# Kernel optimization log

Hardware: AMD Instinct MI355X
Metric: run time of the kernel (lower is better)

The kernel has to match this reference:

```python
import jax, jax.numpy as jnp
import numpy as np

N_NODES = 50000
N_EDGES = 800000
NFEAT = 128
NHID = 128
NCLASS = 10
NUM_GRAPHS = 512


def setup_inputs() -> dict:
    key = jax.random.key(0)
    ks = jax.random.split(key, 12)
    x = jax.random.normal(ks[0], (N_NODES, NFEAT), dtype=jnp.float32)
    edge_index = jax.random.randint(ks[1], (2, N_EDGES), 0, N_NODES, dtype=jnp.int64)
    batch = jnp.sort(jax.random.randint(ks[2], (N_NODES,), 0, NUM_GRAPHS, dtype=jnp.int64))
    def glorot(k, fan_in, fan_out):
        lim = np.sqrt(6.0 / (fan_in + fan_out))
        return jax.random.uniform(k, (fan_in, fan_out), jnp.float32, -lim, lim)
    return {
        "x": x, "edge_index": edge_index, "batch": batch,
        "W0": glorot(ks[3], NFEAT, NHID), "b0": jnp.zeros((NHID,), jnp.float32),
        "W1": glorot(ks[4], NHID, NHID), "b1": jnp.zeros((NHID,), jnp.float32),
        "W2": glorot(ks[5], NHID, NHID), "b2": jnp.zeros((NHID,), jnp.float32),
        "lin_w": glorot(ks[6], NHID, NCLASS), "lin_b": jnp.zeros((NCLASS,), jnp.float32),
    }


def _gcn_norm(edge_index, n):
    # PyG GCNConv: add self-loops, symmetric normalization D^-1/2 A D^-1/2
    loop = jnp.arange(n, dtype=edge_index.dtype)
    src = jnp.concatenate([edge_index[0], loop])  # [E+N]
    dst = jnp.concatenate([edge_index[1], loop])
    deg = jax.ops.segment_sum(jnp.ones_like(dst, dtype=jnp.float32), dst, num_segments=n)
    dis = jnp.where(deg > 0, jax.lax.rsqrt(jnp.maximum(deg, 1.0)), 0.0)
    norm = dis[src] * dis[dst]  # [E+N]
    return src, dst, norm


def _gcn_conv(x, W, b, src, dst, norm, n):
    h = x @ W                              # [N, nhid]
    msg = h[src] * norm[:, None]           # gather + scale, [E+N, nhid]
    out = jax.ops.segment_sum(msg, dst, num_segments=n)
    return out + b


def reference(x, edge_index, batch, W0, b0, W1, b1, W2, b2, lin_w, lin_b):
    n = x.shape[0]
    src, dst, norm = _gcn_norm(edge_index, n)
    h = x
    for (W, b) in ((W0, b0), (W1, b1), (W2, b2)):
        h = jax.nn.relu(_gcn_conv(h, W, b, src, dst, norm, n))
    # global mean pool over graphs
    sums = jax.ops.segment_sum(h, batch, num_segments=NUM_GRAPHS)
    cnts = jax.ops.segment_sum(jnp.ones((n,), jnp.float32), batch, num_segments=NUM_GRAPHS)
    pooled = sums / jnp.maximum(cnts, 1.0)[:, None]  # [G, nhid]
    logits = pooled @ lin_w + lin_b
    return jax.nn.log_softmax(logits, axis=-1)
```

## Files before the change

kernel.cpp:

```cpp
#include <hip/hip_runtime.h>
#include <hip/hip_fp16.h>


#define FEAT 128
#define NCLASS 10
#define NB_MAX 512

typedef _Float16 h8 __attribute__((ext_vector_type(8)));
typedef float f4 __attribute__((ext_vector_type(4)));

__device__ inline int swz(int row, int cbyte) { return row * 256 + (cbyte ^ ((row & 7) << 4)); }

__global__ void __launch_bounds__(256) prep_kernel(const int* __restrict__ ei,
                                                   int* __restrict__ bhist,
                                                   int ne, int nb, int epb, int hb,
                                                   const float* __restrict__ W0,
                                                   const float* __restrict__ W1,
                                                   const float* __restrict__ W2,
                                                   _Float16* __restrict__ Wt, int wtb,
                                                   const int* __restrict__ batch,
                                                   int* __restrict__ gstart, int n, int g) {
  int t = threadIdx.x;
  if (blockIdx.x >= hb + wtb) {
    int i = (blockIdx.x - hb - wtb) * 256 + t;
    if (i >= n) return;
    int bi = batch[i];
    int bp = (i == 0) ? -1 : batch[i - 1];
    for (int q = bp + 1; q <= bi; ++q) gstart[q] = i;
    if (i == n - 1)
      for (int q = bi + 1; q <= g; ++q) gstart[q] = n;
    return;
  }
  if (blockIdx.x >= hb) {
    int i = (blockIdx.x - hb) * 256 + t;
    if (i < 3 * FEAT * FEAT) {
      int l = i / (FEAT * FEAT);
      int r = i - l * (FEAT * FEAT);
      int nn = r >> 7, kk = r & 127;
      const float* W = (l == 0) ? W0 : (l == 1) ? W1 : W2;
      Wt[i] = (_Float16)W[kk * FEAT + nn];
    }
    return;
  }
  __shared__ int lh[NB_MAX];
  for (int i = t; i < nb; i += 256) lh[i] = 0;
  __syncthreads();
  int r0 = blockIdx.x * epb;
  int r1 = min(r0 + epb, ne);
  for (int k = r0 + t; k < r1; k += 256) atomicAdd(&lh[ei[ne + k] >> 7], 1);
  __syncthreads();
  for (int i = t; i < nb; i += 256)
    if (lh[i]) atomicAdd(&bhist[i], lh[i]);
}

__global__ void __launch_bounds__(512) bscan_kernel(const int* __restrict__ bhist,
                                                    int* __restrict__ bstart,
                                                    int* __restrict__ bcur,
                                                    int nb, int ne) {
  __shared__ int sh[512];
  int t = threadIdx.x;
  int v = (t < nb) ? bhist[t] : 0;
  sh[t] = v;
  __syncthreads();
  int x = v;
  for (int d = 1; d < 512; d <<= 1) {
    int y = (t >= d) ? sh[t - d] : 0;
    __syncthreads();
    x += y;
    sh[t] = x;
    __syncthreads();
  }
  if (t < nb) {
    bstart[t] = x - v;
    bcur[t] = x - v;
  }
  if (t == 0) bstart[nb] = ne;
}

__global__ void __launch_bounds__(256) scatter_kernel(const int* __restrict__ ei,
                                                      int* __restrict__ bcur,
                                                      unsigned* __restrict__ buf,
                                                      int ne, int nb, int epb) {
  __shared__ int lh[NB_MAX], lbs[NB_MAX];
  int t = threadIdx.x;
  for (int i = t; i < nb; i += 256) lh[i] = 0;
  __syncthreads();
  int r0 = blockIdx.x * epb;
  int r1 = min(r0 + epb, ne);
  for (int k = r0 + t; k < r1; k += 256) atomicAdd(&lh[ei[ne + k] >> 7], 1);
  __syncthreads();
  for (int i = t; i < nb; i += 256) {
    int c = lh[i];
    lbs[i] = c ? atomicAdd(&bcur[i], c) : 0;
    lh[i] = 0;
  }
  __syncthreads();
  for (int k = r0 + t; k < r1; k += 256) {
    int src = ei[k];
    int dst = ei[ne + k];
    int b = dst >> 7;
    int p = lbs[b] + atomicAdd(&lh[b], 1);
    buf[p] = (unsigned)src | ((unsigned)(dst & 127) << 25);
  }
}

__global__ void __launch_bounds__(256) bucket_build_kernel(const unsigned* __restrict__ buf,
                                                           const int* __restrict__ bstart,
                                                           int4* __restrict__ off4,
                                                           int* __restrict__ oend,
                                                           int* __restrict__ csr,
                                                           float* __restrict__ dis,
                                                           int n, int csize) {
  __shared__ int cnt[512], cur[512], loc[512], sh[128];
  int b = blockIdx.x, t = threadIdx.x;
  int e0 = bstart[b], e1 = bstart[b + 1];
  int pb = ((e0 + 7) & ~7) + 2048 * b;
  for (int i = t; i < 512; i += 256) cnt[i] = 0;
  __syncthreads();
  for (int k = e0 + t; k < e1; k += 256) {
    unsigned u = buf[k];
    int src = (int)(u & 0x1FFFFFFu);
    int d = u >> 25;
    int c = (src >= 3 * csize) ? 3 : (src >= 2 * csize) ? 2 : (src >= csize) ? 1 : 0;
    atomicAdd(&cnt[d * 4 + c], 1);
  }
  __syncthreads();
  int tot = 0;
  if (t < 128) {
    int p0 = (cnt[t * 4 + 0] + 3) & ~3;
    int p1 = (cnt[t * 4 + 1] + 3) & ~3;
    int p2 = (cnt[t * 4 + 2] + 3) & ~3;
    int p3 = (cnt[t * 4 + 3] + 3) & ~3;
    loc[t * 4 + 0] = 0;
    loc[t * 4 + 1] = p0;
    loc[t * 4 + 2] = p0 + p1;
    loc[t * 4 + 3] = p0 + p1 + p2;
    tot = p0 + p1 + p2 + p3;
    sh[t] = tot;
  }
  __syncthreads();
  int x = tot;
  for (int d = 1; d < 128; d <<= 1) {
    int y = (t < 128 && t >= d) ? sh[t - d] : 0;
    __syncthreads();
    if (t < 128) {
      x += y;
      sh[t] = x;
    }
    __syncthreads();
  }
  if (t < 128) {
    int st = pb + x - tot;
    int node = (b << 7) + t;
    int s0 = st + loc[t * 4 + 0], s1 = st + loc[t * 4 + 1];
    int s2 = st + loc[t * 4 + 2], s3 = st + loc[t * 4 + 3];
    cur[t * 4 + 0] = s0;
    cur[t * 4 + 1] = s1;
    cur[t * 4 + 2] = s2;
    cur[t * 4 + 3] = s3;
    if (node < n) {
      off4[node] = make_int4(s0, s1, s2, s3);
      oend[node] = st + tot;
      int v = cnt[t * 4] + cnt[t * 4 + 1] + cnt[t * 4 + 2] + cnt[t * 4 + 3];
      dis[node] = rsqrtf((float)(v + 1));
    }
  }
  __syncthreads();
  for (int k = e0 + t; k < e1; k += 256) {
    unsigned u = buf[k];
    int src = (int)(u & 0x1FFFFFFu);
    int d = u >> 25;
    int c = (src >= 3 * csize) ? 3 : (src >= 2 * csize) ? 2 : (src >= csize) ? 1 : 0;
    int p = atomicAdd(&cur[d * 4 + c], 1);
    csr[p] = src;
  }
  __syncthreads();
  if (t < 128) {
#pragma unroll
    for (int c = 0; c < 4; ++c) {
      int k0 = t * 4 + c;
      int pad = ((cnt[k0] + 3) & ~3) - cnt[k0];
      int base = cur[k0];
      for (int q = 0; q < pad; ++q) csr[base + q] = n;
    }
  }
}

__global__ void __launch_bounds__(256) gemm_mfma_kernel(const float* __restrict__ Xf,
                                                        const _Float16* __restrict__ Wt,
                                                        const float* __restrict__ dis,
                                                        _Float16* __restrict__ Hs, int n) {
  __shared__ _Float16 st[64 * FEAT];
  int tid = threadIdx.x;
  int w = tid >> 6, lane = tid & 63;
  int l15 = lane & 15, hi = lane >> 4;

  int rowA = blockIdx.x * 64 + w * 16 + l15;
  int rA = min(rowA, n - 1);

  f4 acc[8];
#pragma unroll
  for (int nb = 0; nb < 8; ++nb) acc[nb] = (f4)(0.f);

#pragma unroll
  for (int kk = 0; kk < FEAT; kk += 32) {
    int ko = kk + hi * 8;
    h8 a;
    float4 x0 = *(const float4*)&Xf[(size_t)rA * FEAT + ko];
    float4 x1 = *(const float4*)&Xf[(size_t)rA * FEAT + ko + 4];
    a[0] = (_Float16)x0.x; a[1] = (_Float16)x0.y; a[2] = (_Float16)x0.z; a[3] = (_Float16)x0.w;
    a[4] = (_Float16)x1.x; a[5] = (_Float16)x1.y; a[6] = (_Float16)x1.z; a[7] = (_Float16)x1.w;
#pragma unroll
    for (int nb = 0; nb < 8; ++nb) {
      h8 bfr = *(const h8*)&Wt[(nb * 16 + l15) * FEAT + ko];
      acc[nb] = __builtin_amdgcn_mfma_f32_16x16x32_f16(a, bfr, acc[nb], 0, 0, 0);
    }
  }

  float dv[4];
#pragma unroll
  for (int r = 0; r < 4; ++r) {
    int grow = blockIdx.x * 64 + w * 16 + hi * 4 + r;
    dv[r] = dis[min(grow, n - 1)];
  }
#pragma unroll
  for (int nb = 0; nb < 8; ++nb)
#pragma unroll
    for (int r = 0; r < 4; ++r)
      st[(w * 16 + hi * 4 + r) * FEAT + nb * 16 + l15] = (_Float16)(acc[nb][r] * dv[r]);
  __syncthreads();

  int rowbase = blockIdx.x * 64;
#pragma unroll
  for (int i = tid; i < 64 * FEAT / 8; i += 256) {
    int row = rowbase + (i >> 4);
    if (row < n)
      *(uint4*)&Hs[(size_t)row * FEAT + (i & 15) * 8] =
          *(const uint4*)&st[(i >> 4) * FEAT + (i & 15) * 8];
  }
}

__global__ void __launch_bounds__(512, 6) fused_kernel(const h8* __restrict__ Hs_in,
                                                       const int* __restrict__ csr,
                                                       const int4* __restrict__ off4,
                                                       const int* __restrict__ oend,
                                                       const float* __restrict__ dis,
                                                       const float* __restrict__ bias,
                                                       const _Float16* __restrict__ Wt,
                                                       _Float16* __restrict__ Hs_out, int n) {
  __shared__ char xsb[64 * 256];
  int tid = threadIdx.x;
  int w = tid >> 6, lane = tid & 63;
  int grp = lane >> 4, lig = lane & 15;
  int row0 = blockIdx.x * 64;
  int g32 = w * 4 + grp;

  int nd0 = min(row0 + g32 * 2, n - 1);
  int nd1 = min(row0 + g32 * 2 + 1, n - 1);
  int4 o0 = off4[nd0], o1 = off4[nd1];
  int oe0 = oend[nd0], oe1 = oend[nd1];

  float acc0[8], acc1[8];
  h8 sv0 = Hs_in[(size_t)nd0 * 16 + lig];
  h8 sv1 = Hs_in[(size_t)nd1 * 16 + lig];
#pragma unroll
  for (int j = 0; j < 8; ++j) {
    acc0[j] = (float)sv0[j];
    acc1[j] = (float)sv1[j];
  }

#pragma unroll
  for (int c = 0; c < 4; ++c) {
    int s0 = (c == 0) ? o0.x : (c == 1) ? o0.y : (c == 2) ? o0.z : o0.w;
    int e0 = (c == 0) ? o0.y : (c == 1) ? o0.z : (c == 2) ? o0.w : oe0;
    for (int k = s0; k < e0; k += 4) {
      int4 ci = *(const int4*)&csr[k];
      h8 v0 = Hs_in[(size_t)ci.x * 16 + lig];
      h8 v1 = Hs_in[(size_t)ci.y * 16 + lig];
      h8 v2 = Hs_in[(size_t)ci.z * 16 + lig];
      h8 v3 = Hs_in[(size_t)ci.w * 16 + lig];
#pragma unroll
      for (int j = 0; j < 8; ++j)
        acc0[j] += ((float)v0[j] + (float)v1[j]) + ((float)v2[j] + (float)v3[j]);
    }
    int s1 = (c == 0) ? o1.x : (c == 1) ? o1.y : (c == 2) ? o1.z : o1.w;
    int e1 = (c == 0) ? o1.y : (c == 1) ? o1.z : (c == 2) ? o1.w : oe1;
    for (int k = s1; k < e1; k += 4) {
      int4 ci = *(const int4*)&csr[k];
      h8 v0 = Hs_in[(size_t)ci.x * 16 + lig];
      h8 v1 = Hs_in[(size_t)ci.y * 16 + lig];
      h8 v2 = Hs_in[(size_t)ci.z * 16 + lig];
      h8 v3 = Hs_in[(size_t)ci.w * 16 + lig];
#pragma unroll
      for (int j = 0; j < 8; ++j)
        acc1[j] += ((float)v0[j] + (float)v1[j]) + ((float)v2[j] + (float)v3[j]);
    }
    __syncthreads();
  }

  float d0 = dis[nd0], d1 = dis[nd1];
  float4 bb0 = ((const float4*)bias)[lig * 2];
  float4 bb1 = ((const float4*)bias)[lig * 2 + 1];
  float bb[8] = {bb0.x, bb0.y, bb0.z, bb0.w, bb1.x, bb1.y, bb1.z, bb1.w};
  h8 oA, oB;
#pragma unroll
  for (int j = 0; j < 8; ++j) {
    oA[j] = (_Float16)fmaxf(fmaf(d0, acc0[j], bb[j]), 0.f);
    oB[j] = (_Float16)fmaxf(fmaf(d1, acc1[j], bb[j]), 0.f);
  }
  *(h8*)(xsb + swz(g32 * 2, lig * 16)) = oA;
  *(h8*)(xsb + swz(g32 * 2 + 1, lig * 16)) = oB;
  __syncthreads();

  int l15 = lane & 15, hi = lane >> 4;
  int strip = w & 3, ch = w >> 2;
  f4 acc[4];
#pragma unroll
  for (int nb = 0; nb < 4; ++nb) acc[nb] = (f4)(0.f);
#pragma unroll
  for (int kk = 0; kk < FEAT; kk += 32) {
    int ko = kk + hi * 8;
    h8 a = *(const h8*)(xsb + swz(strip * 16 + l15, ko * 2));
#pragma unroll
    for (int nb = 0; nb < 4; ++nb) {
      h8 bfr = *(const h8*)&Wt[(ch * 64 + nb * 16 + l15) * FEAT + ko];
      acc[nb] = __builtin_amdgcn_mfma_f32_16x16x32_f16(a, bfr, acc[nb], 0, 0, 0);
    }
  }

  float dv[4];
#pragma unroll
  for (int r = 0; r < 4; ++r) {
    int grow = row0 + strip * 16 + hi * 4 + r;
    dv[r] = dis[min(grow, n - 1)];
  }
  __syncthreads();
#pragma unroll
  for (int nb = 0; nb < 4; ++nb)
#pragma unroll
    for (int r = 0; r < 4; ++r) {
      int srow = strip * 16 + hi * 4 + r;
      *(_Float16*)(xsb + swz(srow, (ch * 64 + nb * 16 + l15) * 2)) =
          (_Float16)(acc[nb][r] * dv[r]);
    }
  __syncthreads();
#pragma unroll
  for (int i = tid; i < 64 * FEAT / 8; i += 512) {
    int row = row0 + (i >> 4);
    if (row < n)
      *(uint4*)&Hs_out[(size_t)row * FEAT + (i & 15) * 8] =
          *(const uint4*)(xsb + swz(i >> 4, (i & 15) * 16));
  }
}

__global__ void __launch_bounds__(512, 6) agg_kernel(const h8* __restrict__ Hs,
                                                     const int* __restrict__ csr,
                                                     const int4* __restrict__ off4,
                                                     const int* __restrict__ oend,
                                                     const float* __restrict__ dis,
                                                     const float* __restrict__ bias,
                                                     h8* __restrict__ out, int n) {
  int tid = threadIdx.x;
  int g32 = tid >> 4, lig = tid & 15;
  int row0 = blockIdx.x * 64;

  float4 bb0 = ((const float4*)bias)[lig * 2];
  float4 bb1 = ((const float4*)bias)[lig * 2 + 1];
  float bb[8] = {bb0.x, bb0.y, bb0.z, bb0.w, bb1.x, bb1.y, bb1.z, bb1.w};

#pragma unroll
  for (int m = 0; m < 2; ++m) {
    int node = row0 + g32 * 2 + m;
    int nd = min(node, n - 1);
    int s = off4[nd].x;
    int e = oend[nd];
    float a0[8], a1[8];
    h8 sv = Hs[(size_t)nd * 16 + lig];
#pragma unroll
    for (int j = 0; j < 8; ++j) {
      a0[j] = (float)sv[j];
      a1[j] = 0.f;
    }
    for (int k = s; k < e; k += 4) {
      int4 ci = *(const int4*)&csr[k];
      h8 v0 = Hs[(size_t)ci.x * 16 + lig];
      h8 v1 = Hs[(size_t)ci.y * 16 + lig];
      h8 v2 = Hs[(size_t)ci.z * 16 + lig];
      h8 v3 = Hs[(size_t)ci.w * 16 + lig];
#pragma unroll
      for (int j = 0; j < 8; ++j) a0[j] += (float)v0[j] + (float)v2[j];
#pragma unroll
      for (int j = 0; j < 8; ++j) a1[j] += (float)v1[j] + (float)v3[j];
    }
    float d = dis[nd];
    h8 o;
#pragma unroll
    for (int j = 0; j < 8; ++j)
      o[j] = (_Float16)fmaxf(fmaf(d, a0[j] + a1[j], bb[j]), 0.f);
    if (node < n) out[(size_t)node * 16 + lig] = o;
  }
}

__global__ void __launch_bounds__(128) pool_kernel(const __half* __restrict__ h,
                                                   const int* __restrict__ gstart,
                                                   const float* __restrict__ lw,
                                                   const float* __restrict__ lb,
                                                   float* __restrict__ out) {
  int g = blockIdx.x;
  int t = threadIdx.x;
  int s = gstart[g];
  int e = gstart[g + 1];
  float a0 = 0.f, a1 = 0.f, a2 = 0.f, a3 = 0.f;
  int i = s;
  for (; i + 4 <= e; i += 4) {
    a0 += __half2float(h[(size_t)i * FEAT + t]);
    a1 += __half2float(h[(size_t)(i + 1) * FEAT + t]);
    a2 += __half2float(h[(size_t)(i + 2) * FEAT + t]);
    a3 += __half2float(h[(size_t)(i + 3) * FEAT + t]);
  }
  for (; i < e; ++i) a0 += __half2float(h[(size_t)i * FEAT + t]);
  float acc = a0 + a1 + a2 + a3;
  float cnt = (float)(e - s);
  float pooled = acc / fmaxf(cnt, 1.f);
  __shared__ float lds[FEAT];
  __shared__ float logits[NCLASS];
  lds[t] = pooled;
  __syncthreads();
  if (t < NCLASS) {
    float z = lb[t];
    for (int k = 0; k < FEAT; ++k) z += lds[k] * lw[k * NCLASS + t];
    logits[t] = z;
  }
  __syncthreads();
  if (t < NCLASS) {
    float m = logits[0];
#pragma unroll
    for (int c = 1; c < NCLASS; ++c) m = fmaxf(m, logits[c]);
    float ssum = 0.f;
#pragma unroll
    for (int c = 0; c < NCLASS; ++c) ssum += expf(logits[c] - m);
    out[(size_t)g * NCLASS + t] = logits[t] - m - logf(ssum);
  }
}

extern "C" void kernel_launch(void* const* d_in, const int* in_sizes, int n_in,
                              void* d_out, int out_size, void* d_ws, size_t ws_size,
                              hipStream_t stream) {
  const float* x = (const float*)d_in[0];
  const int* ei = (const int*)d_in[1];
  const int* batch = (const int*)d_in[2];
  const float* W0 = (const float*)d_in[3];
  const float* b0 = (const float*)d_in[4];
  const float* W1 = (const float*)d_in[5];
  const float* b1 = (const float*)d_in[6];
  const float* W2 = (const float*)d_in[7];
  const float* b2 = (const float*)d_in[8];
  const float* lw = (const float*)d_in[9];
  const float* lb = (const float*)d_in[10];

  int n = in_sizes[2];
  int ne = in_sizes[1] / 2;
  int g = out_size / NCLASS;
  int nb = (n + 127) >> 7;
  int csize = (n + 3) / 4;
  int hblocks = 120;
  int epb = (ne + hblocks - 1) / hblocks;
  int wtblocks = (3 * FEAT * FEAT + 255) / 256;
  int bndblocks = (n + 255) / 256;

  char* ws = (char*)d_ws;
  size_t p = 0;
  auto alloc = [&](size_t bytes) {
    size_t cur = p;
    p += (bytes + 255) & ~(size_t)255;
    return cur;
  };
  int4* off4 = (int4*)(ws + alloc((size_t)n * 16));
  int* oend = (int*)(ws + alloc((size_t)n * 4));
  int* csr = (int*)(ws + alloc(((size_t)ne + 2048 * (size_t)nb + 64) * 4));
  int* bhist = (int*)(ws + alloc((size_t)NB_MAX * 4));
  int* bstart = (int*)(ws + alloc((size_t)(NB_MAX + 1) * 4));
  int* bcur = (int*)(ws + alloc((size_t)NB_MAX * 4));
  int* gstart = (int*)(ws + alloc((size_t)(g + 1) * 4));
  float* dis = (float*)(ws + alloc((size_t)n * 4));
  unsigned* buf = (unsigned*)(ws + alloc((size_t)ne * 4));
  _Float16* Wt = (_Float16*)(ws + alloc((size_t)3 * FEAT * FEAT * 2));
  _Float16* HA = (_Float16*)(ws + alloc((size_t)(n + 1) * FEAT * 2));
  _Float16* HB = (_Float16*)(ws + alloc((size_t)(n + 1) * FEAT * 2));

  hipMemsetAsync(bhist, 0, NB_MAX * 4, stream);
  hipMemsetAsync(HA + (size_t)n * FEAT, 0, FEAT * 2, stream);
  hipMemsetAsync(HB + (size_t)n * FEAT, 0, FEAT * 2, stream);

  prep_kernel<<<hblocks + wtblocks + bndblocks, 256, 0, stream>>>(
      ei, bhist, ne, nb, epb, hblocks, W0, W1, W2, Wt, wtblocks, batch, gstart, n, g);
  bscan_kernel<<<1, 512, 0, stream>>>(bhist, bstart, bcur, nb, ne);
  scatter_kernel<<<hblocks, 256, 0, stream>>>(ei, bcur, buf, ne, nb, epb);
  bucket_build_kernel<<<nb, 256, 0, stream>>>(buf, bstart, off4, oend, csr, dis, n, csize);

  int gblocks = (n + 63) / 64;
  gemm_mfma_kernel<<<gblocks, 256, 0, stream>>>(x, Wt, dis, HA, n);
  fused_kernel<<<gblocks, 512, 0, stream>>>((const h8*)HA, csr, off4, oend, dis, b0,
                                            Wt + (size_t)1 * FEAT * FEAT, HB, n);
  fused_kernel<<<gblocks, 512, 0, stream>>>((const h8*)HB, csr, off4, oend, dis, b1,
                                            Wt + (size_t)2 * FEAT * FEAT, HA, n);
  agg_kernel<<<gblocks, 512, 0, stream>>>((const h8*)HA, csr, off4, oend, dis, b2,
                                          (h8*)HB, n);

  pool_kernel<<<g, 128, 0, stream>>>((const __half*)HB, gstart, lw, lb, (float*)d_out);
}
```

Measured before the change: 215.2 us.

## Replace histogram+scan bucketing with fixed-capacity buckets and merge memsets into prep

Removes the global edge histogram pass and the single-block scan by giving each destination bucket a fixed capacity region, so scatter's atomic counters directly yield per-bucket counts. The zeroing of counters and padding rows moves into the prep kernel, eliminating separate memset calls. This saves a full read of the destination indices and two launches. The cost is that correctness now assumes no bucket exceeds the fixed capacity, plus extra workspace.

```diff
diff --git a/kernel.cpp b/kernel.cpp
--- a/kernel.cpp
+++ b/kernel.cpp
@@ -5,34 +5,32 @@
 #define FEAT 128
 #define NCLASS 10
 #define NB_MAX 512
+#define BCAP 3072
+#define CSTRIDE 4608
 
 typedef _Float16 h8 __attribute__((ext_vector_type(8)));
 typedef float f4 __attribute__((ext_vector_type(4)));
 
 __device__ inline int swz(int row, int cbyte) { return row * 256 + (cbyte ^ ((row & 7) << 4)); }
 
-__global__ void __launch_bounds__(256) prep_kernel(const int* __restrict__ ei,
-                                                   int* __restrict__ bhist,
-                                                   int ne, int nb, int epb, int hb,
-                                                   const float* __restrict__ W0,
+__global__ void __launch_bounds__(256) prep_kernel(const float* __restrict__ W0,
                                                    const float* __restrict__ W1,
                                                    const float* __restrict__ W2,
                                                    _Float16* __restrict__ Wt, int wtb,
                                                    const int* __restrict__ batch,
-                                                   int* __restrict__ gstart, int n, int g) {
+                                                   int* __restrict__ gstart, int n, int g,
+                                                   int* __restrict__ bcur,
+                                                   unsigned* __restrict__ HA32,
+                                                   unsigned* __restrict__ HB32) {
   int t = threadIdx.x;
-  if (blockIdx.x >= hb + wtb) {
-    int i = (blockIdx.x - hb - wtb) * 256 + t;
-    if (i >= n) return;
-    int bi = batch[i];
-    int bp = (i == 0) ? -1 : batch[i - 1];
-    for (int q = bp + 1; q <= bi; ++q) gstart[q] = i;
-    if (i == n - 1)
-      for (int q = bi + 1; q <= g; ++q) gstart[q] = n;
+  if (blockIdx.x == 0) {
+    for (int i = t; i < NB_MAX; i += 256) bcur[i] = 0;
+    if (t < 64) HA32[(size_t)n * 64 + t] = 0u;
+    else if (t < 128) HB32[(size_t)n * 64 + (t - 64)] = 0u;
     return;
   }
-  if (blockIdx.x >= hb) {
-    int i = (blockIdx.x - hb) * 256 + t;
+  if (blockIdx.x <= wtb) {
+    int i = (blockIdx.x - 1) * 256 + t;
     if (i < 3 * FEAT * FEAT) {
       int l = i / (FEAT * FEAT);
       int r = i - l * (FEAT * FEAT);
@@ -42,39 +40,13 @@
     }
     return;
   }
-  __shared__ int lh[NB_MAX];
-  for (int i = t; i < nb; i += 256) lh[i] = 0;
-  __syncthreads();
-  int r0 = blockIdx.x * epb;
-  int r1 = min(r0 + epb, ne);
-  for (int k = r0 + t; k < r1; k += 256) atomicAdd(&lh[ei[ne + k] >> 7], 1);
-  __syncthreads();
-  for (int i = t; i < nb; i += 256)
-    if (lh[i]) atomicAdd(&bhist[i], lh[i]);
-}
-
-__global__ void __launch_bounds__(512) bscan_kernel(const int* __restrict__ bhist,
-                                                    int* __restrict__ bstart,
-                                                    int* __restrict__ bcur,
-                                                    int nb, int ne) {
-  __shared__ int sh[512];
-  int t = threadIdx.x;
-  int v = (t < nb) ? bhist[t] : 0;
-  sh[t] = v;
-  __syncthreads();
-  int x = v;
-  for (int d = 1; d < 512; d <<= 1) {
-    int y = (t >= d) ? sh[t - d] : 0;
-    __syncthreads();
-    x += y;
-    sh[t] = x;
-    __syncthreads();
-  }
-  if (t < nb) {
-    bstart[t] = x - v;
-    bcur[t] = x - v;
-  }
-  if (t == 0) bstart[nb] = ne;
+  int i = (blockIdx.x - 1 - wtb) * 256 + t;
+  if (i >= n) return;
+  int bi = batch[i];
+  int bp = (i == 0) ? -1 : batch[i - 1];
+  for (int q = bp + 1; q <= bi; ++q) gstart[q] = i;
+  if (i == n - 1)
+    for (int q = bi + 1; q <= g; ++q) gstart[q] = n;
 }
 
 __global__ void __launch_bounds__(256) scatter_kernel(const int* __restrict__ ei,
@@ -100,12 +72,12 @@
     int dst = ei[ne + k];
     int b = dst >> 7;
     int p = lbs[b] + atomicAdd(&lh[b], 1);
-    buf[p] = (unsigned)src | ((unsigned)(dst & 127) << 25);
+    buf[(size_t)b * BCAP + p] = (unsigned)src | ((unsigned)(dst & 127) << 25);
   }
 }
 
 __global__ void __launch_bounds__(256) bucket_build_kernel(const unsigned* __restrict__ buf,
-                                                           const int* __restrict__ bstart,
+                                                           const int* __restrict__ bcnt,
                                                            int4* __restrict__ off4,
                                                            int* __restrict__ oend,
                                                            int* __restrict__ csr,
@@ -113,8 +85,9 @@
                                                            int n, int csize) {
   __shared__ int cnt[512], cur[512], loc[512], sh[128];
   int b = blockIdx.x, t = threadIdx.x;
-  int e0 = bstart[b], e1 = bstart[b + 1];
-  int pb = ((e0 + 7) & ~7) + 2048 * b;
+  int e0 = b * BCAP;
+  int e1 = e0 + bcnt[b];
+  int pb = b * CSTRIDE;
   for (int i = t; i < 512; i += 256) cnt[i] = 0;
   __syncthreads();
   for (int k = e0 + t; k < e1; k += 256) {
@@ -477,26 +450,19 @@
   };
   int4* off4 = (int4*)(ws + alloc((size_t)n * 16));
   int* oend = (int*)(ws + alloc((size_t)n * 4));
-  int* csr = (int*)(ws + alloc(((size_t)ne + 2048 * (size_t)nb + 64) * 4));
-  int* bhist = (int*)(ws + alloc((size_t)NB_MAX * 4));
-  int* bstart = (int*)(ws + alloc((size_t)(NB_MAX + 1) * 4));
+  int* csr = (int*)(ws + alloc((size_t)nb * CSTRIDE * 4));
   int* bcur = (int*)(ws + alloc((size_t)NB_MAX * 4));
   int* gstart = (int*)(ws + alloc((size_t)(g + 1) * 4));
   float* dis = (float*)(ws + alloc((size_t)n * 4));
-  unsigned* buf = (unsigned*)(ws + alloc((size_t)ne * 4));
+  unsigned* buf = (unsigned*)(ws + alloc((size_t)nb * BCAP * 4));
   _Float16* Wt = (_Float16*)(ws + alloc((size_t)3 * FEAT * FEAT * 2));
   _Float16* HA = (_Float16*)(ws + alloc((size_t)(n + 1) * FEAT * 2));
   _Float16* HB = (_Float16*)(ws + alloc((size_t)(n + 1) * FEAT * 2));
 
-  hipMemsetAsync(bhist, 0, NB_MAX * 4, stream);
-  hipMemsetAsync(HA + (size_t)n * FEAT, 0, FEAT * 2, stream);
-  hipMemsetAsync(HB + (size_t)n * FEAT, 0, FEAT * 2, stream);
-
-  prep_kernel<<<hblocks + wtblocks + bndblocks, 256, 0, stream>>>(
-      ei, bhist, ne, nb, epb, hblocks, W0, W1, W2, Wt, wtblocks, batch, gstart, n, g);
-  bscan_kernel<<<1, 512, 0, stream>>>(bhist, bstart, bcur, nb, ne);
+  prep_kernel<<<1 + wtblocks + bndblocks, 256, 0, stream>>>(
+      W0, W1, W2, Wt, wtblocks, batch, gstart, n, g, bcur, (unsigned*)HA, (unsigned*)HB);
   scatter_kernel<<<hblocks, 256, 0, stream>>>(ei, bcur, buf, ne, nb, epb);
-  bucket_build_kernel<<<nb, 256, 0, stream>>>(buf, bstart, off4, oend, csr, dis, n, csize);
+  bucket_build_kernel<<<nb, 256, 0, stream>>>(buf, bcur, off4, oend, csr, dis, n, csize);
 
   int gblocks = (n + 63) / 64;
   gemm_mfma_kernel<<<gblocks, 256, 0, stream>>>(x, Wt, dis, HA, n);
```

After: 201.6 us. 6.3% less time.
